# Kernel optimization log

Hardware: AMD Instinct MI355X
Metric: run time of the kernel (lower is better)

## Reference

```python
import jax, jax.numpy as jnp
import numpy as np

N, E, CIN, COUT, T = 50000, 800000, 64, 64, 12


def setup_inputs() -> dict:
    key = jax.random.key(0)
    k1, k2, k3, k4, k5, k6 = jax.random.split(key, 6)
    x = jax.random.normal(k1, (N, CIN, T), dtype=jnp.float32)
    src = jax.random.randint(k2, (E,), 0, N, dtype=jnp.int32)
    dst = jax.random.randint(k3, (E,), 0, N, dtype=jnp.int32)
    edge_index = jnp.stack([src, dst], axis=0)
    edge_attr = jax.random.uniform(k4, (E,), dtype=jnp.float32)
    W = jax.random.normal(k5, (CIN, COUT), dtype=jnp.float32) / np.sqrt(CIN)
    b = jax.random.normal(k6, (COUT,), dtype=jnp.float32) * 0.01
    return {"x": x, "edge_index": edge_index, "edge_attr": edge_attr, "W": W, "b": b}


def reference(x, edge_index, edge_attr, W, b):
    # GCNConv applied independently to each of T temporal slices, then ReLU.
    n = x.shape[0]
    src, dst = edge_index[0], edge_index[1]
    # add self-loops with weight 1.0 (PyG GCNConv default)
    loop = jnp.arange(n, dtype=src.dtype)
    src_f = jnp.concatenate([src, loop])
    dst_f = jnp.concatenate([dst, loop])
    ew = jnp.concatenate([edge_attr, jnp.ones((n,), x.dtype)])
    # symmetric normalization: deg computed at target (col) nodes
    deg = jax.ops.segment_sum(ew, dst_f, num_segments=n)
    dis = jnp.where(deg > 0, jax.lax.rsqrt(deg), 0.0)
    norm = dis[src_f] * ew * dis[dst_f]  # (E+N,)

    def step(carry, x_t):  # x_t: (N, Cin)
        xw = x_t @ W                              # (N, Cout)
        msgs = xw[src_f] * norm[:, None]          # (E+N, Cout) gather
        out = jax.ops.segment_sum(msgs, dst_f, num_segments=n) + b
        return carry, jax.nn.relu(out)

    _, ys = jax.lax.scan(step, None, jnp.transpose(x, (2, 0, 1)))  # (T, N, Cout)
    return jnp.transpose(ys, (1, 2, 0))  # (N, Cout, T)
```

## Files before the change

kernel.cpp:

```cpp
#include <hip/hip_runtime.h>

#define CIN   64
#define COUT  64
#define TT    12
#define FEAT  (CIN * TT)
#define QROW  (FEAT / 4)

typedef unsigned int uint32;
typedef unsigned long long u64;
typedef float  __attribute__((ext_vector_type(4))) f32x4;

#define DEG_SCALE 1048576.0f

__device__ __forceinline__ void cvt_range(const f32x4* __restrict__ x,
                                          uint2* __restrict__ xh,
                                          int qlo, int qhi, int tid, int stride) {
    for (int i = qlo + tid; i < qhi; i += stride) {
        f32x4 v = __builtin_nontemporal_load(&x[i]);
        uint32 u0 = __float_as_uint(v.x), u1 = __float_as_uint(v.y);
        uint32 u2 = __float_as_uint(v.z), u3 = __float_as_uint(v.w);
        u0 = (u0 + 0x7fffu + ((u0 >> 16) & 1)) >> 16;
        u1 = (u1 + 0x7fffu + ((u1 >> 16) & 1)) >> 16;
        u2 = (u2 + 0x7fffu + ((u2 >> 16) & 1)) >> 16;
        u3 = (u3 + 0x7fffu + ((u3 >> 16) & 1)) >> 16;
        uint2 o; o.x = u0 | (u1 << 16); o.y = u2 | (u3 << 16);
        xh[i] = o;
    }
}

__global__ __launch_bounds__(256) void k_deg_cvt(
    const f32x4* __restrict__ x, uint2* __restrict__ xh, int qlo, int qhi, int nbCvt,
    const int* __restrict__ dst, const float* __restrict__ ea,
    u64* __restrict__ deg64, int e_cnt)
{
    int bid = blockIdx.x;
    if (bid < nbCvt) {
        cvt_range(x, xh, qlo, qhi, bid * 256 + threadIdx.x, nbCvt * 256);
    } else {
        int e = (bid - nbCvt) * 256 + threadIdx.x;
        if (e < e_cnt) {
            u64 v = ((u64)1 << 32) | (u64)(uint32)(ea[e] * DEG_SCALE + 0.5f);
            atomicAdd(&deg64[dst[e]], v);
        }
    }
}

__global__ __launch_bounds__(256) void k_disred(const u64* __restrict__ deg64,
                                                float* __restrict__ dis,
                                                int* __restrict__ partial, int n) {
    __shared__ int red[256];
    int t = threadIdx.x;
    int i = blockIdx.x * 256 + t;
    int cnt = 0;
    if (i < n) {
        u64 v = deg64[i];
        cnt = (int)(v >> 32);
        dis[i] = rsqrtf(1.0f + (float)(uint32)v * (1.0f / DEG_SCALE));
    }
    red[t] = cnt;
    __syncthreads();
    for (int off = 128; off > 0; off >>= 1) {
        if (t < off) red[t] += red[t + off];
        __syncthreads();
    }
    if (t == 0) partial[blockIdx.x] = red[0];
}

__global__ __launch_bounds__(256) void k_scanwrite(const u64* __restrict__ deg64,
                                                   const int* __restrict__ partial,
                                                   int nb,
                                                   int* __restrict__ rowptr,
                                                   int* __restrict__ cursor, int n) {
    __shared__ int tmp[256];
    __shared__ int pred[256];
    int t = threadIdx.x;
    int bid = blockIdx.x;
    int i = bid * 256 + t;

    int pv = (t < nb) ? partial[t] : 0;
    pred[t] = (t < bid) ? pv : 0;
    int v = (i < n) ? (int)(deg64[i] >> 32) : 0;
    tmp[t] = v;
    __syncthreads();
    for (int off = 128; off > 0; off >>= 1) {
        if (t < off) pred[t] += pred[t + off];
        __syncthreads();
    }
    for (int off = 1; off < 256; off <<= 1) {
        int u = (t >= off) ? tmp[t - off] : 0;
        __syncthreads();
        tmp[t] += u;
        __syncthreads();
    }
    int blockOff = pred[0];
    int excl = tmp[t] - v + blockOff;
    if (i < n) { rowptr[i] = excl; cursor[i] = excl; }
    if (bid == nb - 1 && t == 255) rowptr[n] = blockOff + tmp[255];
}

__global__ __launch_bounds__(256) void k_fill_cvt(
    const f32x4* __restrict__ x, uint2* __restrict__ xh, int qlo, int qhi, int nbCvt,
    const int* __restrict__ src, const int* __restrict__ dst,
    const float* __restrict__ ea, const float* __restrict__ dis,
    int* __restrict__ cursor, int2* __restrict__ csr, int e_cnt)
{
    int bid = blockIdx.x;
    if (bid < nbCvt) {
        cvt_range(x, xh, qlo, qhi, bid * 256 + threadIdx.x, nbCvt * 256);
    } else {
        int e = (bid - nbCvt) * 256 + threadIdx.x;
        if (e < e_cnt) {
            int s = src[e], d = dst[e];
            int pos = atomicAdd(&cursor[d], 1);
            float w = dis[s] * ea[e] * dis[d];
            int2 p; p.x = s; p.y = __float_as_int(w);
            csr[pos] = p;
        }
    }
}

template <int BF16>
__global__ __launch_bounds__(192) void k_conv(
    const void* __restrict__ xsrc, const float* __restrict__ W,
    const float* __restrict__ b, const float* __restrict__ dis,
    const int* __restrict__ rowptr, const int2* __restrict__ csr,
    float* __restrict__ out)
{
    __shared__ float sAgg[FEAT];
    __shared__ int2  sE[192];
    __shared__ float sB[COUT];

    const int n = blockIdx.x;
    const int t = threadIdx.x;
    if (t < COUT) sB[t] = b[t];

    const int start = rowptr[n];
    const int end   = rowptr[n + 1];
    const float dn  = dis[n];
    const float selfw = dn * dn;

    float a0, a1, a2, a3;
    if (BF16) {
        const uint2* xb = (const uint2*)xsrc;
        uint2 v = xb[(size_t)n * QROW + t];
        a0 = selfw * __uint_as_float(v.x << 16);
        a1 = selfw * __uint_as_float(v.x & 0xffff0000u);
        a2 = selfw * __uint_as_float(v.y << 16);
        a3 = selfw * __uint_as_float(v.y & 0xffff0000u);
    } else {
        const f32x4* xb = (const f32x4*)xsrc;
        f32x4 v = xb[(size_t)n * QROW + t];
        a0 = selfw * v.x; a1 = selfw * v.y; a2 = selfw * v.z; a3 = selfw * v.w;
    }

    for (int base = start; base < end; base += 192) {
        int cnt = end - base; if (cnt > 192) cnt = 192;
        __syncthreads();
        if (t < cnt) sE[t] = csr[base + t];
        __syncthreads();
        for (int j = 0; j < cnt; ++j) {
            int s    = sE[j].x;
            float w  = __int_as_float(sE[j].y);
            if (BF16) {
                const uint2* xb = (const uint2*)xsrc;
                uint2 v = xb[(size_t)s * QROW + t];
                a0 = fmaf(w, __uint_as_float(v.x << 16),         a0);
                a1 = fmaf(w, __uint_as_float(v.x & 0xffff0000u), a1);
                a2 = fmaf(w, __uint_as_float(v.y << 16),         a2);
                a3 = fmaf(w, __uint_as_float(v.y & 0xffff0000u), a3);
            } else {
                const f32x4* xb = (const f32x4*)xsrc;
                f32x4 v = xb[(size_t)s * QROW + t];
                a0 = fmaf(w, v.x, a0); a1 = fmaf(w, v.y, a1);
                a2 = fmaf(w, v.z, a2); a3 = fmaf(w, v.w, a3);
            }
        }
    }

    float4 av; av.x = a0; av.y = a1; av.z = a2; av.w = a3;
    *((float4*)&sAgg[4 * t]) = av;
    __syncthreads();

    const int co  = t & 63;
    const int tg  = t >> 6;
    const int tt0 = tg * 4;
    float o0 = sB[co], o1 = o0, o2 = o0, o3 = o0;
#pragma unroll
    for (int c = 0; c < CIN; ++c) {
        float wv = W[c * COUT + co];
        o0 = fmaf(wv, sAgg[c * TT + tt0    ], o0);
        o1 = fmaf(wv, sAgg[c * TT + tt0 + 1], o1);
        o2 = fmaf(wv, sAgg[c * TT + tt0 + 2], o2);
        o3 = fmaf(wv, sAgg[c * TT + tt0 + 3], o3);
    }
    o0 = fmaxf(o0, 0.0f); o1 = fmaxf(o1, 0.0f);
    o2 = fmaxf(o2, 0.0f); o3 = fmaxf(o3, 0.0f);

    __syncthreads();
    float4 ov; ov.x = o0; ov.y = o1; ov.z = o2; ov.w = o3;
    *((float4*)&sAgg[co * TT + tt0]) = ov;
    __syncthreads();
    f32x4 r = *((const f32x4*)&sAgg[4 * t]);
    __builtin_nontemporal_store(r, (f32x4*)(out + (size_t)n * FEAT + 4 * t));
}

extern "C" void kernel_launch(void* const* d_in, const int* in_sizes, int n_in,
                              void* d_out, int out_size, void* d_ws, size_t ws_size,
                              hipStream_t stream) {
    const float* x   = (const float*)d_in[0];
    const int*   ei  = (const int*)d_in[1];
    const float* ea  = (const float*)d_in[2];
    const float* W   = (const float*)d_in[3];
    const float* b   = (const float*)d_in[4];
    float* out = (float*)d_out;

    const int E = in_sizes[2];
    const int N = in_sizes[0] / FEAT;
    const int* src = ei;
    const int* dst = ei + E;

    size_t off = 0;
    char* ws = (char*)d_ws;
    auto alloc = [&](size_t bytes) -> char* {
        char* p = ws + off;
        off = (off + bytes + 15) & ~(size_t)15;
        return p;
    };
    u64*   deg64   = (u64*)  alloc((size_t)N * 8);
    float* dis     = (float*)alloc((size_t)N * 4);
    int*   rowptr  = (int*)  alloc((size_t)(N + 1) * 4);
    int*   cursor  = (int*)  alloc((size_t)N * 4);
    int*   partial = (int*)  alloc(4096);
    int2*  csr     = (int2*) alloc((size_t)E * 8);
    unsigned short* xh = (unsigned short*)alloc((size_t)N * FEAT * 2);
    const bool use_bf16 = (off <= ws_size);

    int nb_n   = (N + 255) / 256;
    int nb_e   = (E + 255) / 256;
    int nquads = (N * FEAT) / 4;
    int halfQ  = nquads / 2;
    int nbCvt  = use_bf16 ? 1024 : 0;

    (void)hipMemsetAsync(deg64, 0, (size_t)N * 8, stream);
    k_deg_cvt  <<<nbCvt + nb_e, 256, 0, stream>>>((const f32x4*)x, (uint2*)xh,
                                                  0, halfQ, nbCvt, dst, ea, deg64, E);
    k_disred   <<<nb_n, 256, 0, stream>>>(deg64, dis, partial, N);
    k_scanwrite<<<nb_n, 256, 0, stream>>>(deg64, partial, nb_n, rowptr, cursor, N);
    k_fill_cvt <<<nbCvt + nb_e, 256, 0, stream>>>((const f32x4*)x, (uint2*)xh,
                                                  halfQ, nquads, nbCvt,
                                                  src, dst, ea, dis, cursor, csr, E);
    if (use_bf16)
        k_conv<1><<<N, 192, 0, stream>>>(xh, W, b, dis, rowptr, csr, out);
    else
        k_conv<0><<<N, 192, 0, stream>>>(x,  W, b, dis, rowptr, csr, out);
}
```

Measured before the change: 311.1 us.

## Transpose bf16 features into time-split halves and run conv in two passes

The fp32-to-bf16 conversion now also transposes each node's features so that timesteps 0-5 and 6-11 live in separate contiguous halves of the row. Aggregation is split into two launches, each covering one half. Each pass gathers a smaller working set (half the feature bytes per neighbor), which is meant to improve L2/cache hit rates on the random neighbor gathers. The cost is a second pass over the CSR edges, a second launch, and the W matmul running twice with half the work each.

Result: slower. 445.4 us (+43.2%).

```diff
diff --git a/kernel.cpp b/kernel.cpp
--- a/kernel.cpp
+++ b/kernel.cpp
@@ -4,38 +4,54 @@
 #define COUT  64
 #define TT    12
 #define FEAT  (CIN * TT)
-#define QROW  (FEAT / 4)
+#define UROW  (FEAT / 2)
+#define UPASS 192
 
 typedef unsigned int uint32;
 typedef unsigned long long u64;
 typedef float  __attribute__((ext_vector_type(4))) f32x4;
+typedef float  __attribute__((ext_vector_type(2))) f32x2;
 
 #define DEG_SCALE 1048576.0f
 
-__device__ __forceinline__ void cvt_range(const f32x4* __restrict__ x,
-                                          uint2* __restrict__ xh,
-                                          int qlo, int qhi, int tid, int stride) {
-    for (int i = qlo + tid; i < qhi; i += stride) {
-        f32x4 v = __builtin_nontemporal_load(&x[i]);
-        uint32 u0 = __float_as_uint(v.x), u1 = __float_as_uint(v.y);
-        uint32 u2 = __float_as_uint(v.z), u3 = __float_as_uint(v.w);
-        u0 = (u0 + 0x7fffu + ((u0 >> 16) & 1)) >> 16;
-        u1 = (u1 + 0x7fffu + ((u1 >> 16) & 1)) >> 16;
-        u2 = (u2 + 0x7fffu + ((u2 >> 16) & 1)) >> 16;
-        u3 = (u3 + 0x7fffu + ((u3 >> 16) & 1)) >> 16;
-        uint2 o; o.x = u0 | (u1 << 16); o.y = u2 | (u3 << 16);
-        xh[i] = o;
+__device__ __forceinline__ uint32 bf16rne(float f) {
+    uint32 u = __float_as_uint(f);
+    return (u + 0x7fffu + ((u >> 16) & 1)) >> 16;
+}
+__device__ __forceinline__ uint32 pk(float lo, float hi) {
+    return bf16rne(lo) | (bf16rne(hi) << 16);
+}
+
+__device__ __forceinline__ void cvtT_range(const float* __restrict__ x,
+                                           uint32* __restrict__ xh2,
+                                           int lo, int hi, int tid, int stride) {
+    for (int idx = lo + tid; idx < hi; idx += stride) {
+        int n = idx >> 5, m = idx & 31;
+        const f32x4* s = (const f32x4*)(x + (size_t)n * FEAT + m * 24);
+        f32x4 q0 = __builtin_nontemporal_load(&s[0]);
+        f32x4 q1 = __builtin_nontemporal_load(&s[1]);
+        f32x4 q2 = __builtin_nontemporal_load(&s[2]);
+        f32x4 q3 = __builtin_nontemporal_load(&s[3]);
+        f32x4 q4 = __builtin_nontemporal_load(&s[4]);
+        f32x4 q5 = __builtin_nontemporal_load(&s[5]);
+        uint32* d = xh2 + (size_t)n * UROW + m;
+        d[0 * 32] = pk(q0.x, q3.x);  d[1 * 32] = pk(q0.y, q3.y);
+        d[2 * 32] = pk(q0.z, q3.z);  d[3 * 32] = pk(q0.w, q3.w);
+        d[4 * 32] = pk(q1.x, q4.x);  d[5 * 32] = pk(q1.y, q4.y);
+        d[6 * 32] = pk(q1.z, q4.z);  d[7 * 32] = pk(q1.w, q4.w);
+        d[8 * 32] = pk(q2.x, q5.x);  d[9 * 32] = pk(q2.y, q5.y);
+        d[10 * 32] = pk(q2.z, q5.z); d[11 * 32] = pk(q2.w, q5.w);
     }
 }
 
 __global__ __launch_bounds__(256) void k_deg_cvt(
-    const f32x4* __restrict__ x, uint2* __restrict__ xh, int qlo, int qhi, int nbCvt,
+    const float* __restrict__ x, uint32* __restrict__ xh2, int ulo, int uhi, int nbCvt,
     const int* __restrict__ dst, const float* __restrict__ ea,
     u64* __restrict__ deg64, int e_cnt)
 {
     int bid = blockIdx.x;
     if (bid < nbCvt) {
-        cvt_range(x, xh, qlo, qhi, bid * 256 + threadIdx.x, nbCvt * 256);
+        cvtT_range(x, xh2, ulo, uhi, bid * 256 + threadIdx.x, nbCvt * 256);
     } else {
         int e = (bid - nbCvt) * 256 + threadIdx.x;
         if (e < e_cnt) {
@@ -99,14 +115,14 @@
 }
 
 __global__ __launch_bounds__(256) void k_fill_cvt(
-    const f32x4* __restrict__ x, uint2* __restrict__ xh, int qlo, int qhi, int nbCvt,
+    const float* __restrict__ x, uint32* __restrict__ xh2, int ulo, int uhi, int nbCvt,
     const int* __restrict__ src, const int* __restrict__ dst,
     const float* __restrict__ ea, const float* __restrict__ dis,
     int* __restrict__ cursor, int2* __restrict__ csr, int e_cnt)
 {
     int bid = blockIdx.x;
     if (bid < nbCvt) {
-        cvt_range(x, xh, qlo, qhi, bid * 256 + threadIdx.x, nbCvt * 256);
+        cvtT_range(x, xh2, ulo, uhi, bid * 256 + threadIdx.x, nbCvt * 256);
     } else {
         int e = (bid - nbCvt) * 256 + threadIdx.x;
         if (e < e_cnt) {
@@ -119,9 +135,63 @@
     }
 }
 
-template <int BF16>
-__global__ __launch_bounds__(192) void k_conv(
-    const void* __restrict__ xsrc, const float* __restrict__ W,
+__global__ __launch_bounds__(192) void k_conv2(
+    const uint32* __restrict__ xh2, const float* __restrict__ W,
+    const float* __restrict__ b, const float* __restrict__ dis,
+    const int* __restrict__ rowptr, const int2* __restrict__ csr,
+    float* __restrict__ out, int pass)
+{
+    __shared__ float sAgg[2 * UPASS];
+    __shared__ int2  sE[192];
+    __shared__ float sB[COUT];
+
+    const int n = blockIdx.x;
+    const int t = threadIdx.x;
+    if (t < COUT) sB[t] = b[t];
+
+    const int start = rowptr[n];
+    const int end   = rowptr[n + 1];
+    const float dn  = dis[n];
+    const float selfw = dn * dn;
+
+    const uint32* xb = xh2 + pass * UPASS;
+    uint32 v = xb[(size_t)n * UROW + t];
+    float a0 = selfw * __uint_as_float(v << 16);
+    float a1 = selfw * __uint_as_float(v & 0xffff0000u);
+
+    for (int base = start; base < end; base += 192) {
+        int cnt = end - base; if (cnt > 192) cnt = 192;
+        __syncthreads();
+        if (t < cnt) sE[t] = csr[base + t];
+        __syncthreads();
+        for (int j = 0; j < cnt; ++j) {
+            int s    = sE[j].x;
+            float w  = __int_as_float(sE[j].y);
+            uint32 u = xb[(size_t)s * UROW + t];
+            a0 = fmaf(w, __uint_as_float(u << 16),         a0);
+            a1 = fmaf(w, __uint_as_float(u & 0xffff0000u), a1);
+        }
+    }
+
+    f32x2 av; av.x = a0; av.y = a1;
+    *((f32x2*)&sAgg[2 * t]) = av;
+    __syncthreads();
+
+    const int co = t & 63;
+    const int tg = t >> 6;
+    float o0 = sB[co], o1 = sB[co];
+#pragma unroll
+    for (int c = 0; c < CIN; ++c) {
+        float wv = W[c * COUT + co];
+        o0 = fmaf(wv, sAgg[(tg * 2    ) * 64 + c], o0);
+        o1 = fmaf(wv, sAgg[(tg * 2 + 1) * 64 + c], o1);
+    }
+    f32x2 r; r.x = fmaxf(o0, 0.0f); r.y = fmaxf(o1, 0.0f);
+    *((f32x2*)(out + (size_t)n * FEAT + co * TT + pass * 6 + tg * 2)) = r;
+}
+
+__global__ __launch_bounds__(192) void k_conv_f32(
+    const float* __restrict__ xsrc, const float* __restrict__ W,
     const float* __restrict__ b, const float* __restrict__ dis,
     const int* __restrict__ rowptr, const int2* __restrict__ csr,
     float* __restrict__ out)
@@ -139,19 +209,9 @@
     const float dn  = dis[n];
     const float selfw = dn * dn;
 
-    float a0, a1, a2, a3;
-    if (BF16) {
-        const uint2* xb = (const uint2*)xsrc;
-        uint2 v = xb[(size_t)n * QROW + t];
-        a0 = selfw * __uint_as_float(v.x << 16);
-        a1 = selfw * __uint_as_float(v.x & 0xffff0000u);
-        a2 = selfw * __uint_as_float(v.y << 16);
-        a3 = selfw * __uint_as_float(v.y & 0xffff0000u);
-    } else {
-        const f32x4* xb = (const f32x4*)xsrc;
-        f32x4 v = xb[(size_t)n * QROW + t];
-        a0 = selfw * v.x; a1 = selfw * v.y; a2 = selfw * v.z; a3 = selfw * v.w;
-    }
+    const f32x4* xb = (const f32x4*)xsrc;
+    f32x4 v = xb[(size_t)n * (FEAT / 4) + t];
+    float a0 = selfw * v.x, a1 = selfw * v.y, a2 = selfw * v.z, a3 = selfw * v.w;
 
     for (int base = start; base < end; base += 192) {
         int cnt = end - base; if (cnt > 192) cnt = 192;
@@ -161,19 +221,9 @@
         for (int j = 0; j < cnt; ++j) {
             int s    = sE[j].x;
             float w  = __int_as_float(sE[j].y);
-            if (BF16) {
-                const uint2* xb = (const uint2*)xsrc;
-                uint2 v = xb[(size_t)s * QROW + t];
-                a0 = fmaf(w, __uint_as_float(v.x << 16),         a0);
-                a1 = fmaf(w, __uint_as_float(v.x & 0xffff0000u), a1);
-                a2 = fmaf(w, __uint_as_float(v.y << 16),         a2);
-                a3 = fmaf(w, __uint_as_float(v.y & 0xffff0000u), a3);
-            } else {
-                const f32x4* xb = (const f32x4*)xsrc;
-                f32x4 v = xb[(size_t)s * QROW + t];
-                a0 = fmaf(w, v.x, a0); a1 = fmaf(w, v.y, a1);
-                a2 = fmaf(w, v.z, a2); a3 = fmaf(w, v.w, a3);
-            }
+            f32x4 u = xb[(size_t)s * (FEAT / 4) + t];
+            a0 = fmaf(w, u.x, a0); a1 = fmaf(w, u.y, a1);
+            a2 = fmaf(w, u.z, a2); a3 = fmaf(w, u.w, a3);
         }
     }
 
@@ -232,25 +282,26 @@
     int*   cursor  = (int*)  alloc((size_t)N * 4);
     int*   partial = (int*)  alloc(4096);
     int2*  csr     = (int2*) alloc((size_t)E * 8);
-    unsigned short* xh = (unsigned short*)alloc((size_t)N * FEAT * 2);
+    uint32* xh2    = (uint32*)alloc((size_t)N * FEAT * 2);
     const bool use_bf16 = (off <= ws_size);
 
     int nb_n   = (N + 255) / 256;
     int nb_e   = (E + 255) / 256;
-    int nquads = (N * FEAT) / 4;
-    int halfQ  = nquads / 2;
+    int nunits = N * 32;
+    int halfU  = nunits / 2;
     int nbCvt  = use_bf16 ? 1024 : 0;
 
     (void)hipMemsetAsync(deg64, 0, (size_t)N * 8, stream);
-    k_deg_cvt  <<<nbCvt + nb_e, 256, 0, stream>>>((const f32x4*)x, (uint2*)xh,
-                                                  0, halfQ, nbCvt, dst, ea, deg64, E);
+    k_deg_cvt  <<<nbCvt + nb_e, 256, 0, stream>>>(x, xh2, 0, halfU, nbCvt,
+                                                  dst, ea, deg64, E);
     k_disred   <<<nb_n, 256, 0, stream>>>(deg64, dis, partial, N);
     k_scanwrite<<<nb_n, 256, 0, stream>>>(deg64, partial, nb_n, rowptr, cursor, N);
-    k_fill_cvt <<<nbCvt + nb_e, 256, 0, stream>>>((const f32x4*)x, (uint2*)xh,
-                                                  halfQ, nquads, nbCvt,
+    k_fill_cvt <<<nbCvt + nb_e, 256, 0, stream>>>(x, xh2, halfU, nunits, nbCvt,
                                                   src, dst, ea, dis, cursor, csr, E);
-    if (use_bf16)
-        k_conv<1><<<N, 192, 0, stream>>>(xh, W, b, dis, rowptr, csr, out);
-    else
-        k_conv<0><<<N, 192, 0, stream>>>(x,  W, b, dis, rowptr, csr, out);
-}
+    if (use_bf16) {
+        k_conv2<<<N, 192, 0, stream>>>(xh2, W, b, dis, rowptr, csr, out, 0);
+        k_conv2<<<N, 192, 0, stream>>>(xh2, W, b, dis, rowptr, csr, out, 1);
+    } else {
+        k_conv_f32<<<N, 192, 0, stream>>>(x, W, b, dis, rowptr, csr, out);
+    }
+}
```
